# Optimization experiments

Measured on AMD Instinct MI355X. Metric: run time of the kernel, lower is better.

## Reference

```python
import jax, jax.numpy as jnp
import numpy as np

B, TOPK, MN = 128, 32, 64
MAX_NODES, H, E = 256, 128, 128
N_ENT, N_REL = 40000, 400


def setup_inputs() -> dict:
    key = jax.random.key(0)
    ks = jax.random.split(key, 11)
    s = 0.02  # weight init scale
    return {
        "node_embeddings": jax.random.normal(ks[0], (B, MAX_NODES + 2, H), jnp.float32),
        "entity_table": jax.random.normal(ks[1], (N_ENT, E), jnp.float32) * s,
        "relation_table": jax.random.normal(ks[2], (N_REL, E), jnp.float32) * s,
        "W_ih": jax.random.normal(ks[3], (3 * H, 2 * E), jnp.float32) * s,
        "W_hh": jax.random.normal(ks[4], (3 * H, H), jnp.float32) * s,
        "b_ih": jax.random.normal(ks[5], (3 * H,), jnp.float32) * s,
        "b_hh": jax.random.normal(ks[6], (3 * H,), jnp.float32) * s,
        "aim_nodes": jax.random.randint(ks[7], (B, TOPK), 0, MAX_NODES),
        "aim_entities": jax.random.randint(ks[8], (B, TOPK), 0, N_ENT),
        "neighbors": jax.random.randint(ks[9], (B, TOPK, MN, 2), 0, MAX_NODES + 2),
        "neighbors_num": jax.random.randint(ks[10], (B, TOPK), 0, MN + 1),
    }


def reference(node_embeddings, entity_table, relation_table, W_ih, W_hh, b_ih, b_hh,
              aim_nodes, aim_entities, neighbors, neighbors_num):
    # Agent.aggregate with use_rnn=True; returns updated node_embeddings.
    b, topk, mn, _ = neighbors.shape
    h_dim = node_embeddings.shape[-1]
    nb_nodes = neighbors[..., 0]      # (B, topk, mn) node positions
    nb_rel = neighbors[..., 1]        # (B, topk, mn) relation ids

    # per-batch gather of hidden states of neighbor nodes -> (B, topk, mn, H)
    h = jnp.take_along_axis(node_embeddings,
                            nb_nodes.reshape(b, topk * mn)[:, :, None],
                            axis=1).reshape(b, topk, mn, h_dim)
    ent = entity_table[aim_entities]          # (B, topk, E)
    rel = relation_table[nb_rel]              # (B, topk, mn, E)
    # GRU input: concat(aim entity embedding broadcast over neighbors, relation emb)
    x = jnp.concatenate(
        [jnp.broadcast_to(ent[:, :, None, :], rel.shape), rel], axis=-1)  # (B,topk,mn,2E)

    # torch GRUCell: gates ordered (r, z, n)
    gi = jnp.einsum('btme,ge->btmg', x, W_ih) + b_ih  # (B,topk,mn,3H)
    gh = jnp.einsum('btmh,gh->btmg', h, W_hh) + b_hh
    i_r, i_z, i_n = jnp.split(gi, 3, axis=-1)
    h_r, h_z, h_n = jnp.split(gh, 3, axis=-1)
    r = jax.nn.sigmoid(i_r + h_r)
    z = jax.nn.sigmoid(i_z + h_z)
    n = jnp.tanh(i_n + r * h_n)
    h_new = (1.0 - z) * n + z * h              # (B,topk,mn,H)

    # masked mean over valid neighbors (masked_fill(0) then sum / max(num,1))
    mask = jnp.arange(mn)[None, None, :] < neighbors_num[:, :, None]
    denom = neighbors_num.astype(h_new.dtype) + (neighbors_num == 0).astype(h_new.dtype)
    upd = jnp.where(mask[..., None], h_new, 0.0).sum(axis=2) / denom[..., None]  # (B,topk,H)

    # scatter updated representations back into the node table
    bidx = jnp.arange(b)[:, None]
    return node_embeddings.at[bidx, aim_nodes].set(upd)
```

## Files before the change

### kernel.cpp

```cpp
#include <hip/hip_runtime.h>

#define BB     128
#define TOPK   32
#define MN     64
#define NODES  258
#define HD     128
#define G3     384
#define NREL   400
#define SEG1_OFF 448
#define SEG2_OFF 4544
#define NROWS_TOT 37568
#define ROWPAD   37632
#define COLSPLIT 3

typedef __bf16 bf16x8 __attribute__((ext_vector_type(8)));
typedef float  f32x4  __attribute__((ext_vector_type(4)));

__device__ inline unsigned short f2bf(float f) {
    unsigned u = __float_as_uint(f);
    u = (u + 0x7fff + ((u >> 16) & 1)) >> 16;
    return (unsigned short)u;
}
__device__ inline float bf2f(unsigned short s) {
    return __uint_as_float(((unsigned)s) << 16);
}
__device__ inline float fsig(float x) {
    float e = __builtin_amdgcn_exp2f(-1.442695041f * x);
    return __builtin_amdgcn_rcpf(1.f + e);
}
__device__ inline float ftanh(float x) {
    x = fminf(15.f, fmaxf(-15.f, x));
    float e = __builtin_amdgcn_exp2f(2.885390082f * x);
    return (e - 1.f) * __builtin_amdgcn_rcpf(e + 1.f);
}

__global__ __launch_bounds__(256) void pack_all(
        const float* __restrict__ node_emb, const float* __restrict__ ent_tab,
        const float* __restrict__ rel_tab, const int* __restrict__ aim_ent,
        unsigned short* __restrict__ A, float* __restrict__ out) {
    int i = blockIdx.x * 256 + threadIdx.x;
    int row = i >> 4, kc = (i & 15) << 3;
    float4 v0 = {0.f,0.f,0.f,0.f}, v1 = {0.f,0.f,0.f,0.f};
    if (row < NREL) {
        const float4* p = (const float4*)(rel_tab + (size_t)row * 128 + kc);
        v0 = p[0]; v1 = p[1];
    } else if (row < SEG1_OFF) {
    } else if (row < SEG2_OFF) {
        const float* e = ent_tab + (size_t)aim_ent[row - SEG1_OFF] * 128 + kc;
        v0 = ((const float4*)e)[0]; v1 = ((const float4*)e)[1];
    } else if (row < NROWS_TOT) {
        int n = row - SEG2_OFF;
        const float4* p = (const float4*)(node_emb + (size_t)n * 128 + kc);
        v0 = p[0]; v1 = p[1];
        float4* o = (float4*)(out + (size_t)n * 128 + kc);
        o[0] = v0; o[1] = v1;
    }
    union { unsigned short s[8]; uint4 v; } u;
    u.s[0]=f2bf(v0.x); u.s[1]=f2bf(v0.y); u.s[2]=f2bf(v0.z); u.s[3]=f2bf(v0.w);
    u.s[4]=f2bf(v1.x); u.s[5]=f2bf(v1.y); u.s[6]=f2bf(v1.z); u.s[7]=f2bf(v1.w);
    *(uint4*)(A + (size_t)row * 128 + kc) = u.v;
}

__global__ __launch_bounds__(256) void pack_w(
        const float* __restrict__ W_ih, const float* __restrict__ W_hh,
        const float* __restrict__ b_ih, const float* __restrict__ b_hh,
        unsigned short* __restrict__ Wpack, float* __restrict__ biasb) {
    int i = blockIdx.x * 256 + threadIdx.x;
    int s = i / 49152, r = i % 49152;
    int n = r >> 7, k = r & 127;
    float v;
    if (s == 0)      v = W_ih[n * 256 + 128 + k];
    else if (s == 1) v = W_ih[n * 256 + k];
    else             v = W_hh[n * 128 + k];
    Wpack[i] = f2bf(v);
    if (i < 3 * 384) {
        int s2 = i / 384, g = i % 384;
        biasb[i] = (s2 == 0) ? 0.f : (s2 == 1 ? b_ih[g] : b_hh[g]);
    }
}

__global__ __launch_bounds__(256) void mfma_gemm(
        const unsigned short* __restrict__ A, const unsigned short* __restrict__ Wpack,
        const float* __restrict__ biasb, unsigned short* __restrict__ G) {
    __shared__ __align__(16) unsigned short Bs[128 * 128];
    const int tid = threadIdx.x;
    const int w = tid >> 6, lane = tid & 63;
    const int rb = blockIdx.x / COLSPLIT, cs = blockIdx.x % COLSPLIT;
    const int row0 = rb * 128 + w * 32;
    const int seg  = (row0 < SEG1_OFF) ? 0 : (row0 < SEG2_OFF ? 1 : 2);
    const int limit = (seg == 0) ? NREL : NROWS_TOT;
    const int colbase = cs * 128;
    const unsigned short* Wt = Wpack + (size_t)seg * 49152 + (size_t)colbase * 128;

#pragma unroll
    for (int ii = 0; ii < 8; ++ii) {
        int dst = ii * 256 + tid;
        int g = dst >> 6, rem = dst & 63;
        int qq = rem >> 4, cc = rem & 15;
        int tt = g >> 2, kbb = g & 3;
        uint4 v = *(const uint4*)(Wt + (size_t)(tt * 16 + cc) * 128 + kbb * 32 + qq * 8);
        *(uint4*)(Bs + dst * 8) = v;
    }

    const int q = lane >> 4, c = lane & 15;
    const int koff = q << 3;
    bf16x8 a0[4], a1[4];
    {
        const unsigned short* Ar0 = A + (size_t)(row0 + c) * 128 + koff;
        const unsigned short* Ar1 = Ar0 + 16 * 128;
#pragma unroll
        for (int kb = 0; kb < 4; ++kb) {
            a0[kb] = *(const bf16x8*)(Ar0 + kb * 32);
            a1[kb] = *(const bf16x8*)(Ar1 + kb * 32);
        }
    }
    float bv[8];
#pragma unroll
    for (int t = 0; t < 8; ++t)
        bv[t] = biasb[seg * 384 + colbase + t * 16 + c];

    __syncthreads();

    const int r0 = row0 + q * 4, r1 = r0 + 16;
#pragma unroll 2
    for (int t = 0; t < 8; ++t) {
        bf16x8 bf[4];
#pragma unroll
        for (int kb = 0; kb < 4; ++kb)
            bf[kb] = *(const bf16x8*)(Bs + (size_t)((t * 4 + kb) * 64 + lane) * 8);
        f32x4 acc0 = {0.f,0.f,0.f,0.f}, acc1 = {0.f,0.f,0.f,0.f};
#pragma unroll
        for (int kb = 0; kb < 4; ++kb) {
            acc0 = __builtin_amdgcn_mfma_f32_16x16x32_bf16(a0[kb], bf[kb], acc0, 0, 0, 0);
            acc1 = __builtin_amdgcn_mfma_f32_16x16x32_bf16(a1[kb], bf[kb], acc1, 0, 0, 0);
        }
        const int gc = colbase + t * 16 + c;
#pragma unroll
        for (int i2 = 0; i2 < 4; ++i2) {
            if (r0 + i2 < limit) G[(size_t)(r0 + i2) * 384 + gc] = f2bf(acc0[i2] + bv[t]);
            if (r1 + i2 < limit) G[(size_t)(r1 + i2) * 384 + gc] = f2bf(acc1[i2] + bv[t]);
        }
    }
}

__global__ __launch_bounds__(128) void gru_agg(
        const float* __restrict__ node_emb, const unsigned short* __restrict__ G,
        const int* __restrict__ aim_nodes, const int* __restrict__ neighbors,
        const int* __restrict__ nb_num, float* __restrict__ out) {
    const int bt = blockIdx.x;
    const int b = bt >> 5, t = bt & 31;
    const int h = threadIdx.x;

    const int myaim = aim_nodes[bt];
    for (int t2 = t + 1; t2 < TOPK; ++t2)
        if (aim_nodes[b * TOPK + t2] == myaim) return;

    __shared__ int2 nbs[MN];
    if (h < MN) nbs[h] = ((const int2*)(neighbors + (size_t)bt * MN * 2))[h];
    __syncthreads();

    const size_t erow = (size_t)(SEG1_OFF + bt) * 384;
    const float ge_r = bf2f(G[erow + h]);
    const float ge_z = bf2f(G[erow + 128 + h]);
    const float ge_n = bf2f(G[erow + 256 + h]);

    int num = nb_num[bt];
    num = (num < 0) ? 0 : (num > MN ? MN : num);

    const unsigned short* ghb = G + (size_t)(SEG2_OFF + b * NODES) * 384;
    const float* heb = node_emb + (size_t)b * NODES * 128;

    float acc = 0.f;
    int m = 0;
    for (; m + 4 <= num; m += 4) {
        float gr_r[4], gr_z[4], gr_n[4], h_r[4], h_z[4], h_n[4], hv[4];
#pragma unroll
        for (int j = 0; j < 4; ++j) {
            int2 p = nbs[m + j];
            const unsigned short* gr = G + (size_t)p.y * 384;
            const unsigned short* gh = ghb + (size_t)p.x * 384;
            gr_r[j] = bf2f(gr[h]); gr_z[j] = bf2f(gr[128 + h]); gr_n[j] = bf2f(gr[256 + h]);
            h_r[j]  = bf2f(gh[h]); h_z[j]  = bf2f(gh[128 + h]); h_n[j]  = bf2f(gh[256 + h]);
            hv[j]   = heb[(size_t)p.x * 128 + h];
        }
#pragma unroll
        for (int j = 0; j < 4; ++j) {
            float r = fsig(ge_r + gr_r[j] + h_r[j]);
            float z = fsig(ge_z + gr_z[j] + h_z[j]);
            float n = ftanh(ge_n + gr_n[j] + r * h_n[j]);
            acc += (1.f - z) * n + z * hv[j];
        }
    }
    for (; m < num; ++m) {
        int2 p = nbs[m];
        const unsigned short* gr = G + (size_t)p.y * 384;
        const unsigned short* gh = ghb + (size_t)p.x * 384;
        float r = fsig(ge_r + bf2f(gr[h]) + bf2f(gh[h]));
        float z = fsig(ge_z + bf2f(gr[128 + h]) + bf2f(gh[128 + h]));
        float n = ftanh(ge_n + bf2f(gr[256 + h]) + r * bf2f(gh[256 + h]));
        acc += (1.f - z) * n + z * heb[(size_t)p.x * 128 + h];
    }
    const float denom = (num > 0) ? (float)num : 1.f;
    out[((size_t)b * NODES + myaim) * 128 + h] = acc * __builtin_amdgcn_rcpf(denom);
}

extern "C" void kernel_launch(void* const* d_in, const int* in_sizes, int n_in,
                              void* d_out, int out_size, void* d_ws, size_t ws_size,
                              hipStream_t stream) {
    const float* node_emb = (const float*)d_in[0];
    const float* ent_tab  = (const float*)d_in[1];
    const float* rel_tab  = (const float*)d_in[2];
    const float* W_ih     = (const float*)d_in[3];
    const float* W_hh     = (const float*)d_in[4];
    const float* b_ih     = (const float*)d_in[5];
    const float* b_hh     = (const float*)d_in[6];
    const int* aim_nodes  = (const int*)d_in[7];
    const int* aim_ent    = (const int*)d_in[8];
    const int* neighbors  = (const int*)d_in[9];
    const int* nb_num     = (const int*)d_in[10];
    float* out = (float*)d_out;

    unsigned short* G     = (unsigned short*)d_ws;
    unsigned short* A     = G + (size_t)NROWS_TOT * 384;
    unsigned short* Wpack = A + (size_t)ROWPAD * 128;
    float*          biasb = (float*)(Wpack + 3 * 384 * 128);

    hipLaunchKernelGGL(pack_all, dim3(ROWPAD * 16 / 256), dim3(256), 0, stream,
                       node_emb, ent_tab, rel_tab, aim_ent, A, out);
    hipLaunchKernelGGL(pack_w, dim3(3 * 384 * 128 / 256), dim3(256), 0, stream,
                       W_ih, W_hh, b_ih, b_hh, Wpack, biasb);
    hipLaunchKernelGGL(mfma_gemm, dim3((ROWPAD / 128) * COLSPLIT), dim3(256), 0, stream,
                       A, Wpack, biasb, G);
    hipLaunchKernelGGL(gru_agg, dim3(BB * TOPK), dim3(128), 0, stream,
                       node_emb, G, aim_nodes, neighbors, nb_num, out);
}
```

Measured before the change: 151.3 us.

## Split GRU neighbor loop across four thread groups and read bf16 hidden states

The GRU aggregation kernel grows from 128 to 512 threads per block. Each 128-thread group handles every fourth neighbor, and the partial sums are combined through shared memory. This exposes more memory-level parallelism in the latency-bound gathers. The node embeddings are also written to a bf16 copy during packing, so the per-neighbor hidden-state read is halved, at the cost of extra rounding in the z*h term. Segment offsets are realigned to 128-row boundaries so each GEMM block selects a single weight segment.

```diff
diff --git a/kernel.cpp b/kernel.cpp
--- a/kernel.cpp
+++ b/kernel.cpp
@@ -7,9 +7,9 @@
 #define HD     128
 #define G3     384
 #define NREL   400
-#define SEG1_OFF 448
-#define SEG2_OFF 4544
-#define NROWS_TOT 37568
+#define SEG1_OFF 512
+#define SEG2_OFF 4608
+#define NROWS_TOT 37632
 #define ROWPAD   37632
 #define COLSPLIT 3
 
@@ -37,10 +37,13 @@
 __global__ __launch_bounds__(256) void pack_all(
         const float* __restrict__ node_emb, const float* __restrict__ ent_tab,
         const float* __restrict__ rel_tab, const int* __restrict__ aim_ent,
-        unsigned short* __restrict__ A, float* __restrict__ out) {
+        unsigned short* __restrict__ A, unsigned short* __restrict__ NE16,
+        float* __restrict__ out) {
     int i = blockIdx.x * 256 + threadIdx.x;
     int row = i >> 4, kc = (i & 15) << 3;
     float4 v0 = {0.f,0.f,0.f,0.f}, v1 = {0.f,0.f,0.f,0.f};
+    bool isnode = false;
+    int n = 0;
     if (row < NREL) {
         const float4* p = (const float4*)(rel_tab + (size_t)row * 128 + kc);
         v0 = p[0]; v1 = p[1];
@@ -48,8 +51,9 @@
     } else if (row < SEG2_OFF) {
         const float* e = ent_tab + (size_t)aim_ent[row - SEG1_OFF] * 128 + kc;
         v0 = ((const float4*)e)[0]; v1 = ((const float4*)e)[1];
-    } else if (row < NROWS_TOT) {
-        int n = row - SEG2_OFF;
+    } else {
+        isnode = true;
+        n = row - SEG2_OFF;
         const float4* p = (const float4*)(node_emb + (size_t)n * 128 + kc);
         v0 = p[0]; v1 = p[1];
         float4* o = (float4*)(out + (size_t)n * 128 + kc);
@@ -59,6 +63,7 @@
     u.s[0]=f2bf(v0.x); u.s[1]=f2bf(v0.y); u.s[2]=f2bf(v0.z); u.s[3]=f2bf(v0.w);
     u.s[4]=f2bf(v1.x); u.s[5]=f2bf(v1.y); u.s[6]=f2bf(v1.z); u.s[7]=f2bf(v1.w);
     *(uint4*)(A + (size_t)row * 128 + kc) = u.v;
+    if (isnode) *(uint4*)(NE16 + (size_t)n * 128 + kc) = u.v;
 }
 
 __global__ __launch_bounds__(256) void pack_w(
@@ -86,8 +91,9 @@
     const int tid = threadIdx.x;
     const int w = tid >> 6, lane = tid & 63;
     const int rb = blockIdx.x / COLSPLIT, cs = blockIdx.x % COLSPLIT;
-    const int row0 = rb * 128 + w * 32;
-    const int seg  = (row0 < SEG1_OFF) ? 0 : (row0 < SEG2_OFF ? 1 : 2);
+    const int brow = rb * 128;
+    const int row0 = brow + w * 32;
+    const int seg  = (brow < SEG1_OFF) ? 0 : (brow < SEG2_OFF ? 1 : 2);
     const int limit = (seg == 0) ? NREL : NROWS_TOT;
     const int colbase = cs * 128;
     const unsigned short* Wt = Wpack + (size_t)seg * 49152 + (size_t)colbase * 128;
@@ -143,20 +149,22 @@
     }
 }
 
-__global__ __launch_bounds__(128) void gru_agg(
-        const float* __restrict__ node_emb, const unsigned short* __restrict__ G,
+__global__ __launch_bounds__(512) void gru_agg(
+        const unsigned short* __restrict__ NE16, const unsigned short* __restrict__ G,
         const int* __restrict__ aim_nodes, const int* __restrict__ neighbors,
         const int* __restrict__ nb_num, float* __restrict__ out) {
     const int bt = blockIdx.x;
     const int b = bt >> 5, t = bt & 31;
-    const int h = threadIdx.x;
+    const int tid = threadIdx.x;
+    const int h = tid & 127, j = tid >> 7;
 
     const int myaim = aim_nodes[bt];
     for (int t2 = t + 1; t2 < TOPK; ++t2)
         if (aim_nodes[b * TOPK + t2] == myaim) return;
 
     __shared__ int2 nbs[MN];
-    if (h < MN) nbs[h] = ((const int2*)(neighbors + (size_t)bt * MN * 2))[h];
+    __shared__ float part[4][128];
+    if (tid < MN) nbs[tid] = ((const int2*)(neighbors + (size_t)bt * MN * 2))[tid];
     __syncthreads();
 
     const size_t erow = (size_t)(SEG1_OFF + bt) * 384;
@@ -168,40 +176,47 @@
     num = (num < 0) ? 0 : (num > MN ? MN : num);
 
     const unsigned short* ghb = G + (size_t)(SEG2_OFF + b * NODES) * 384;
-    const float* heb = node_emb + (size_t)b * NODES * 128;
+    const unsigned short* heb = NE16 + (size_t)b * NODES * 128;
 
     float acc = 0.f;
-    int m = 0;
-    for (; m + 4 <= num; m += 4) {
-        float gr_r[4], gr_z[4], gr_n[4], h_r[4], h_z[4], h_n[4], hv[4];
-#pragma unroll
-        for (int j = 0; j < 4; ++j) {
-            int2 p = nbs[m + j];
-            const unsigned short* gr = G + (size_t)p.y * 384;
-            const unsigned short* gh = ghb + (size_t)p.x * 384;
-            gr_r[j] = bf2f(gr[h]); gr_z[j] = bf2f(gr[128 + h]); gr_n[j] = bf2f(gr[256 + h]);
-            h_r[j]  = bf2f(gh[h]); h_z[j]  = bf2f(gh[128 + h]); h_n[j]  = bf2f(gh[256 + h]);
-            hv[j]   = heb[(size_t)p.x * 128 + h];
-        }
-#pragma unroll
-        for (int j = 0; j < 4; ++j) {
-            float r = fsig(ge_r + gr_r[j] + h_r[j]);
-            float z = fsig(ge_z + gr_z[j] + h_z[j]);
-            float n = ftanh(ge_n + gr_n[j] + r * h_n[j]);
-            acc += (1.f - z) * n + z * hv[j];
-        }
-    }
-    for (; m < num; ++m) {
+    int m = j;
+    for (; m + 4 < num; m += 8) {
+        int2 p0 = nbs[m], p1 = nbs[m + 4];
+        const unsigned short* gr0 = G + (size_t)p0.y * 384;
+        const unsigned short* gh0 = ghb + (size_t)p0.x * 384;
+        const unsigned short* gr1 = G + (size_t)p1.y * 384;
+        const unsigned short* gh1 = ghb + (size_t)p1.x * 384;
+        float ar0 = bf2f(gr0[h]), az0 = bf2f(gr0[128+h]), an0 = bf2f(gr0[256+h]);
+        float hr0 = bf2f(gh0[h]), hz0 = bf2f(gh0[128+h]), hn0 = bf2f(gh0[256+h]);
+        float hv0 = bf2f(heb[(size_t)p0.x * 128 + h]);
+        float ar1 = bf2f(gr1[h]), az1 = bf2f(gr1[128+h]), an1 = bf2f(gr1[256+h]);
+        float hr1 = bf2f(gh1[h]), hz1 = bf2f(gh1[128+h]), hn1 = bf2f(gh1[256+h]);
+        float hv1 = bf2f(heb[(size_t)p1.x * 128 + h]);
+        float r0 = fsig(ge_r + ar0 + hr0);
+        float z0 = fsig(ge_z + az0 + hz0);
+        float n0 = ftanh(ge_n + an0 + r0 * hn0);
+        acc += (1.f - z0) * n0 + z0 * hv0;
+        float r1 = fsig(ge_r + ar1 + hr1);
+        float z1 = fsig(ge_z + az1 + hz1);
+        float n1 = ftanh(ge_n + an1 + r1 * hn1);
+        acc += (1.f - z1) * n1 + z1 * hv1;
+    }
+    if (m < num) {
         int2 p = nbs[m];
         const unsigned short* gr = G + (size_t)p.y * 384;
         const unsigned short* gh = ghb + (size_t)p.x * 384;
         float r = fsig(ge_r + bf2f(gr[h]) + bf2f(gh[h]));
         float z = fsig(ge_z + bf2f(gr[128 + h]) + bf2f(gh[128 + h]));
         float n = ftanh(ge_n + bf2f(gr[256 + h]) + r * bf2f(gh[256 + h]));
-        acc += (1.f - z) * n + z * heb[(size_t)p.x * 128 + h];
-    }
-    const float denom = (num > 0) ? (float)num : 1.f;
-    out[((size_t)b * NODES + myaim) * 128 + h] = acc * __builtin_amdgcn_rcpf(denom);
+        acc += (1.f - z) * n + z * bf2f(heb[(size_t)p.x * 128 + h]);
+    }
+    part[j][h] = acc;
+    __syncthreads();
+    if (j == 0) {
+        float s = part[0][h] + part[1][h] + part[2][h] + part[3][h];
+        const float denom = (num > 0) ? (float)num : 1.f;
+        out[((size_t)b * NODES + myaim) * 128 + h] = s * __builtin_amdgcn_rcpf(denom);
+    }
 }
 
 extern "C" void kernel_launch(void* const* d_in, const int* in_sizes, int n_in,
@@ -222,15 +237,16 @@
 
     unsigned short* G     = (unsigned short*)d_ws;
     unsigned short* A     = G + (size_t)NROWS_TOT * 384;
-    unsigned short* Wpack = A + (size_t)ROWPAD * 128;
+    unsigned short* NE16  = A + (size_t)ROWPAD * 128;
+    unsigned short* Wpack = NE16 + (size_t)BB * NODES * 128;
     float*          biasb = (float*)(Wpack + 3 * 384 * 128);
 
     hipLaunchKernelGGL(pack_all, dim3(ROWPAD * 16 / 256), dim3(256), 0, stream,
-                       node_emb, ent_tab, rel_tab, aim_ent, A, out);
+                       node_emb, ent_tab, rel_tab, aim_ent, A, NE16, out);
     hipLaunchKernelGGL(pack_w, dim3(3 * 384 * 128 / 256), dim3(256), 0, stream,
                        W_ih, W_hh, b_ih, b_hh, Wpack, biasb);
     hipLaunchKernelGGL(mfma_gemm, dim3((ROWPAD / 128) * COLSPLIT), dim3(256), 0, stream,
                        A, Wpack, biasb, G);
-    hipLaunchKernelGGL(gru_agg, dim3(BB * TOPK), dim3(128), 0, stream,
-                       node_emb, G, aim_nodes, neighbors, nb_num, out);
-}
+    hipLaunchKernelGGL(gru_agg, dim3(BB * TOPK), dim3(512), 0, stream,
+                       NE16, G, aim_nodes, neighbors, nb_num, out);
+}
```

New measurement: 151.2 us. No clear change (-0.1%).

## Fuse node hidden-gate GEMM into GRU aggregation kernel using LDS, merge prep kernels

Applied to the files above, without the earlier changes.

Removes the large global GEMM over all node rows. Each block now computes the W_hh projections for one batch's 258 nodes and a 32-column slice of every gate with MFMA, keeping the results in shared memory instead of writing and re-reading a big bf16 G buffer. The two packing kernels become one launch, and the GEMM kernel now only covers relation and entity rows. The per-node hidden state is read from the bf16 packed A rather than fp32 node_emb, which adds a small precision loss, and the W_hh GEMM work is repeated across the four column-quarter blocks.

```diff
diff --git a/kernel.cpp b/kernel.cpp
--- a/kernel.cpp
+++ b/kernel.cpp
@@ -4,14 +4,13 @@
 #define TOPK   32
 #define MN     64
 #define NODES  258
-#define HD     128
-#define G3     384
+#define NPAD   272
 #define NREL   400
-#define SEG1_OFF 448
-#define SEG2_OFF 4544
-#define NROWS_TOT 37568
-#define ROWPAD   37632
-#define COLSPLIT 3
+#define SEG1_OFF 512
+#define SEG2_OFF 4608
+#define NROWS_TOT 37632
+#define NG_ROWS  4608
+#define GH_STRIDE 102
 
 typedef __bf16 bf16x8 __attribute__((ext_vector_type(8)));
 typedef float  f32x4  __attribute__((ext_vector_type(4)));
@@ -34,61 +33,72 @@
     return (e - 1.f) * __builtin_amdgcn_rcpf(e + 1.f);
 }
 
-__global__ __launch_bounds__(256) void pack_all(
+#define REGA_BLOCKS (NROWS_TOT * 16 / 256)
+#define REGB_BLOCKS (147456 / 8 / 256)
+__global__ __launch_bounds__(256) void prep(
         const float* __restrict__ node_emb, const float* __restrict__ ent_tab,
         const float* __restrict__ rel_tab, const int* __restrict__ aim_ent,
-        unsigned short* __restrict__ A, float* __restrict__ out) {
-    int i = blockIdx.x * 256 + threadIdx.x;
-    int row = i >> 4, kc = (i & 15) << 3;
-    float4 v0 = {0.f,0.f,0.f,0.f}, v1 = {0.f,0.f,0.f,0.f};
-    if (row < NREL) {
-        const float4* p = (const float4*)(rel_tab + (size_t)row * 128 + kc);
-        v0 = p[0]; v1 = p[1];
-    } else if (row < SEG1_OFF) {
-    } else if (row < SEG2_OFF) {
-        const float* e = ent_tab + (size_t)aim_ent[row - SEG1_OFF] * 128 + kc;
-        v0 = ((const float4*)e)[0]; v1 = ((const float4*)e)[1];
-    } else if (row < NROWS_TOT) {
-        int n = row - SEG2_OFF;
-        const float4* p = (const float4*)(node_emb + (size_t)n * 128 + kc);
-        v0 = p[0]; v1 = p[1];
-        float4* o = (float4*)(out + (size_t)n * 128 + kc);
-        o[0] = v0; o[1] = v1;
-    }
-    union { unsigned short s[8]; uint4 v; } u;
-    u.s[0]=f2bf(v0.x); u.s[1]=f2bf(v0.y); u.s[2]=f2bf(v0.z); u.s[3]=f2bf(v0.w);
-    u.s[4]=f2bf(v1.x); u.s[5]=f2bf(v1.y); u.s[6]=f2bf(v1.z); u.s[7]=f2bf(v1.w);
-    *(uint4*)(A + (size_t)row * 128 + kc) = u.v;
-}
-
-__global__ __launch_bounds__(256) void pack_w(
         const float* __restrict__ W_ih, const float* __restrict__ W_hh,
         const float* __restrict__ b_ih, const float* __restrict__ b_hh,
-        unsigned short* __restrict__ Wpack, float* __restrict__ biasb) {
-    int i = blockIdx.x * 256 + threadIdx.x;
-    int s = i / 49152, r = i % 49152;
-    int n = r >> 7, k = r & 127;
-    float v;
-    if (s == 0)      v = W_ih[n * 256 + 128 + k];
-    else if (s == 1) v = W_ih[n * 256 + k];
-    else             v = W_hh[n * 128 + k];
-    Wpack[i] = f2bf(v);
-    if (i < 3 * 384) {
-        int s2 = i / 384, g = i % 384;
-        biasb[i] = (s2 == 0) ? 0.f : (s2 == 1 ? b_ih[g] : b_hh[g]);
-    }
-}
-
-__global__ __launch_bounds__(256) void mfma_gemm(
+        unsigned short* __restrict__ A, unsigned short* __restrict__ Wpack,
+        float* __restrict__ biasb, float* __restrict__ out) {
+    int gid = blockIdx.x * 256 + threadIdx.x;
+    if (blockIdx.x < REGA_BLOCKS) {
+        int row = gid >> 4, kc = (gid & 15) << 3;
+        float4 v0 = {0.f,0.f,0.f,0.f}, v1 = {0.f,0.f,0.f,0.f};
+        if (row < NREL) {
+            const float4* p = (const float4*)(rel_tab + (size_t)row * 128 + kc);
+            v0 = p[0]; v1 = p[1];
+        } else if (row < SEG1_OFF) {
+        } else if (row < SEG2_OFF) {
+            const float* e = ent_tab + (size_t)aim_ent[row - SEG1_OFF] * 128 + kc;
+            v0 = ((const float4*)e)[0]; v1 = ((const float4*)e)[1];
+        } else {
+            int n = row - SEG2_OFF;
+            const float4* p = (const float4*)(node_emb + (size_t)n * 128 + kc);
+            v0 = p[0]; v1 = p[1];
+            float4* o = (float4*)(out + (size_t)n * 128 + kc);
+            o[0] = v0; o[1] = v1;
+        }
+        union { unsigned short s[8]; uint4 v; } u;
+        u.s[0]=f2bf(v0.x); u.s[1]=f2bf(v0.y); u.s[2]=f2bf(v0.z); u.s[3]=f2bf(v0.w);
+        u.s[4]=f2bf(v1.x); u.s[5]=f2bf(v1.y); u.s[6]=f2bf(v1.z); u.s[7]=f2bf(v1.w);
+        *(uint4*)(A + (size_t)row * 128 + kc) = u.v;
+    } else {
+        int rb = gid - REGA_BLOCKS * 256;
+        int e0 = rb * 8;
+        int s = e0 / 49152, r = e0 % 49152;
+        int n = r >> 7, k = r & 127;
+        const float* src = (s == 0) ? (W_ih + n * 256 + 128 + k)
+                         : (s == 1) ? (W_ih + n * 256 + k)
+                                    : (W_hh + n * 128 + k);
+        float4 v0 = ((const float4*)src)[0], v1 = ((const float4*)src)[1];
+        union { unsigned short s[8]; uint4 v; } u;
+        u.s[0]=f2bf(v0.x); u.s[1]=f2bf(v0.y); u.s[2]=f2bf(v0.z); u.s[3]=f2bf(v0.w);
+        u.s[4]=f2bf(v1.x); u.s[5]=f2bf(v1.y); u.s[6]=f2bf(v1.z); u.s[7]=f2bf(v1.w);
+        *(uint4*)(Wpack + e0) = u.v;
+        if (rb < 144) {
+            for (int j = 0; j < 8; ++j) {
+                int e = rb * 8 + j;
+                int s2 = e / 384, g = e % 384;
+                biasb[e] = (s2 == 0) ? 0.f : (s2 == 1 ? b_ih[g] : b_hh[g]);
+            }
+        }
+    }
+}
+
+#define COLSPLIT 3
+__global__ __launch_bounds__(256) void mfma_small(
         const unsigned short* __restrict__ A, const unsigned short* __restrict__ Wpack,
-        const float* __restrict__ biasb, unsigned short* __restrict__ G) {
+        const float* __restrict__ biasb, unsigned short* __restrict__ Gs) {
     __shared__ __align__(16) unsigned short Bs[128 * 128];
     const int tid = threadIdx.x;
     const int w = tid >> 6, lane = tid & 63;
     const int rb = blockIdx.x / COLSPLIT, cs = blockIdx.x % COLSPLIT;
-    const int row0 = rb * 128 + w * 32;
-    const int seg  = (row0 < SEG1_OFF) ? 0 : (row0 < SEG2_OFF ? 1 : 2);
-    const int limit = (seg == 0) ? NREL : NROWS_TOT;
+    const int brow = rb * 128;
+    const int row0 = brow + w * 32;
+    const int seg  = (brow < SEG1_OFF) ? 0 : 1;
+    const int limit = (seg == 0) ? NREL : NG_ROWS;
     const int colbase = cs * 128;
     const unsigned short* Wt = Wpack + (size_t)seg * 49152 + (size_t)colbase * 128;
 
@@ -137,71 +147,108 @@
         const int gc = colbase + t * 16 + c;
 #pragma unroll
         for (int i2 = 0; i2 < 4; ++i2) {
-            if (r0 + i2 < limit) G[(size_t)(r0 + i2) * 384 + gc] = f2bf(acc0[i2] + bv[t]);
-            if (r1 + i2 < limit) G[(size_t)(r1 + i2) * 384 + gc] = f2bf(acc1[i2] + bv[t]);
-        }
-    }
-}
-
-__global__ __launch_bounds__(128) void gru_agg(
-        const float* __restrict__ node_emb, const unsigned short* __restrict__ G,
+            if (r0 + i2 < limit) Gs[(size_t)(r0 + i2) * 384 + gc] = f2bf(acc0[i2] + bv[t]);
+            if (r1 + i2 < limit) Gs[(size_t)(r1 + i2) * 384 + gc] = f2bf(acc1[i2] + bv[t]);
+        }
+    }
+}
+
+__global__ __launch_bounds__(512) void fused_gru(
+        const unsigned short* __restrict__ A, const unsigned short* __restrict__ Wpack,
+        const unsigned short* __restrict__ Gs, const float* __restrict__ b_hh,
         const int* __restrict__ aim_nodes, const int* __restrict__ neighbors,
         const int* __restrict__ nb_num, float* __restrict__ out) {
-    const int bt = blockIdx.x;
-    const int b = bt >> 5, t = bt & 31;
-    const int h = threadIdx.x;
-
-    const int myaim = aim_nodes[bt];
-    for (int t2 = t + 1; t2 < TOPK; ++t2)
-        if (aim_nodes[b * TOPK + t2] == myaim) return;
-
-    __shared__ int2 nbs[MN];
-    if (h < MN) nbs[h] = ((const int2*)(neighbors + (size_t)bt * MN * 2))[h];
+    __shared__ __align__(16) unsigned short gh[NPAD * GH_STRIDE];
+    const int b = blockIdx.x & 127, quart = blockIdx.x >> 7;
+    const int h0 = quart * 32;
+    const int tid = threadIdx.x, w = tid >> 6, lane = tid & 63;
+    const unsigned short* An = A + ((size_t)SEG2_OFF + (size_t)b * NODES) * 128;
+
+    const int q = lane >> 4, c = lane & 15;
+    const int koff = q << 3;
+    const unsigned short* W2 = Wpack + 2 * 49152;
+    for (int rt = w; rt < 17; rt += 8) {
+        int ar = rt * 16 + c;
+        int arc = (ar < NODES) ? ar : 0;
+        bf16x8 af[4];
+#pragma unroll
+        for (int kb = 0; kb < 4; ++kb)
+            af[kb] = *(const bf16x8*)(An + (size_t)arc * 128 + kb * 32 + koff);
+#pragma unroll
+        for (int ct = 0; ct < 6; ++ct) {
+            int gate = ct >> 1, sub = ct & 1;
+            int gc = gate * 128 + h0 + sub * 16 + c;
+            bf16x8 bf[4];
+#pragma unroll
+            for (int kb = 0; kb < 4; ++kb)
+                bf[kb] = *(const bf16x8*)(W2 + (size_t)gc * 128 + kb * 32 + koff);
+            f32x4 acc = {0.f,0.f,0.f,0.f};
+#pragma unroll
+            for (int kb = 0; kb < 4; ++kb)
+                acc = __builtin_amdgcn_mfma_f32_16x16x32_bf16(af[kb], bf[kb], acc, 0, 0, 0);
+            float bias = b_hh[gc];
+            int col = gate * 32 + sub * 16 + c;
+#pragma unroll
+            for (int i2 = 0; i2 < 4; ++i2) {
+                int row = rt * 16 + q * 4 + i2;
+                gh[row * GH_STRIDE + col] = f2bf(acc[i2] + bias);
+            }
+        }
+    }
     __syncthreads();
 
-    const size_t erow = (size_t)(SEG1_OFF + bt) * 384;
-    const float ge_r = bf2f(G[erow + h]);
-    const float ge_z = bf2f(G[erow + 128 + h]);
-    const float ge_n = bf2f(G[erow + 256 + h]);
-
-    int num = nb_num[bt];
-    num = (num < 0) ? 0 : (num > MN ? MN : num);
-
-    const unsigned short* ghb = G + (size_t)(SEG2_OFF + b * NODES) * 384;
-    const float* heb = node_emb + (size_t)b * NODES * 128;
-
-    float acc = 0.f;
-    int m = 0;
-    for (; m + 4 <= num; m += 4) {
-        float gr_r[4], gr_z[4], gr_n[4], h_r[4], h_z[4], h_n[4], hv[4];
-#pragma unroll
-        for (int j = 0; j < 4; ++j) {
-            int2 p = nbs[m + j];
-            const unsigned short* gr = G + (size_t)p.y * 384;
-            const unsigned short* gh = ghb + (size_t)p.x * 384;
-            gr_r[j] = bf2f(gr[h]); gr_z[j] = bf2f(gr[128 + h]); gr_n[j] = bf2f(gr[256 + h]);
-            h_r[j]  = bf2f(gh[h]); h_z[j]  = bf2f(gh[128 + h]); h_n[j]  = bf2f(gh[256 + h]);
-            hv[j]   = heb[(size_t)p.x * 128 + h];
-        }
-#pragma unroll
-        for (int j = 0; j < 4; ++j) {
-            float r = fsig(ge_r + gr_r[j] + h_r[j]);
-            float z = fsig(ge_z + gr_z[j] + h_z[j]);
-            float n = ftanh(ge_n + gr_n[j] + r * h_n[j]);
-            acc += (1.f - z) * n + z * hv[j];
-        }
-    }
-    for (; m < num; ++m) {
-        int2 p = nbs[m];
-        const unsigned short* gr = G + (size_t)p.y * 384;
-        const unsigned short* gh = ghb + (size_t)p.x * 384;
-        float r = fsig(ge_r + bf2f(gr[h]) + bf2f(gh[h]));
-        float z = fsig(ge_z + bf2f(gr[128 + h]) + bf2f(gh[128 + h]));
-        float n = ftanh(ge_n + bf2f(gr[256 + h]) + r * bf2f(gh[256 + h]));
-        acc += (1.f - z) * n + z * heb[(size_t)p.x * 128 + h];
-    }
-    const float denom = (num > 0) ? (float)num : 1.f;
-    out[((size_t)b * NODES + myaim) * 128 + h] = acc * __builtin_amdgcn_rcpf(denom);
+    const int half = lane >> 5, hh = lane & 31;
+    for (int ti = 0; ti < 2; ++ti) {
+        const int t = w * 4 + ti * 2 + half;
+        const int bt = b * TOPK + t;
+        const int aim = aim_nodes[bt];
+        bool wr = true;
+        for (int t2 = t + 1; t2 < TOPK; ++t2)
+            if (aim_nodes[b * TOPK + t2] == aim) wr = false;
+        int num = nb_num[bt];
+        num = (num < 0) ? 0 : (num > MN ? MN : num);
+        const int2* nb = (const int2*)neighbors + (size_t)bt * MN;
+        const size_t erow = (size_t)(SEG1_OFF + bt) * 384;
+        const float ge_r = bf2f(Gs[erow + h0 + hh]);
+        const float ge_z = bf2f(Gs[erow + 128 + h0 + hh]);
+        const float ge_n = bf2f(Gs[erow + 256 + h0 + hh]);
+
+        float acc = 0.f;
+        int m = 0;
+        for (; m + 2 <= num; m += 2) {
+            int2 p0 = nb[m], p1 = nb[m + 1];
+            const unsigned short* gr0 = Gs + (size_t)p0.y * 384 + h0;
+            const unsigned short* gr1 = Gs + (size_t)p1.y * 384 + h0;
+            const unsigned short* g0 = gh + p0.x * GH_STRIDE;
+            const unsigned short* g1 = gh + p1.x * GH_STRIDE;
+            float a_r0 = bf2f(gr0[hh]),  a_z0 = bf2f(gr0[128 + hh]), a_n0 = bf2f(gr0[256 + hh]);
+            float h_r0 = bf2f(g0[hh]),   h_z0 = bf2f(g0[32 + hh]),   h_n0 = bf2f(g0[64 + hh]);
+            float hv0  = bf2f(An[(size_t)p0.x * 128 + h0 + hh]);
+            float a_r1 = bf2f(gr1[hh]),  a_z1 = bf2f(gr1[128 + hh]), a_n1 = bf2f(gr1[256 + hh]);
+            float h_r1 = bf2f(g1[hh]),   h_z1 = bf2f(g1[32 + hh]),   h_n1 = bf2f(g1[64 + hh]);
+            float hv1  = bf2f(An[(size_t)p1.x * 128 + h0 + hh]);
+            float r0 = fsig(ge_r + a_r0 + h_r0);
+            float z0 = fsig(ge_z + a_z0 + h_z0);
+            float n0 = ftanh(ge_n + a_n0 + r0 * h_n0);
+            acc += (1.f - z0) * n0 + z0 * hv0;
+            float r1 = fsig(ge_r + a_r1 + h_r1);
+            float z1 = fsig(ge_z + a_z1 + h_z1);
+            float n1 = ftanh(ge_n + a_n1 + r1 * h_n1);
+            acc += (1.f - z1) * n1 + z1 * hv1;
+        }
+        if (m < num) {
+            int2 p = nb[m];
+            const unsigned short* gr = Gs + (size_t)p.y * 384 + h0;
+            const unsigned short* g0 = gh + p.x * GH_STRIDE;
+            float r = fsig(ge_r + bf2f(gr[hh]) + bf2f(g0[hh]));
+            float z = fsig(ge_z + bf2f(gr[128 + hh]) + bf2f(g0[32 + hh]));
+            float n = ftanh(ge_n + bf2f(gr[256 + hh]) + r * bf2f(g0[64 + hh]));
+            acc += (1.f - z) * n + z * bf2f(An[(size_t)p.x * 128 + h0 + hh]);
+        }
+        const float denom = (num > 0) ? (float)num : 1.f;
+        if (wr)
+            out[((size_t)b * NODES + aim) * 128 + h0 + hh] = acc * __builtin_amdgcn_rcpf(denom);
+    }
 }
 
 extern "C" void kernel_launch(void* const* d_in, const int* in_sizes, int n_in,
@@ -220,17 +267,16 @@
     const int* nb_num     = (const int*)d_in[10];
     float* out = (float*)d_out;
 
-    unsigned short* G     = (unsigned short*)d_ws;
-    unsigned short* A     = G + (size_t)NROWS_TOT * 384;
-    unsigned short* Wpack = A + (size_t)ROWPAD * 128;
+    unsigned short* Gs    = (unsigned short*)d_ws;
+    unsigned short* A     = Gs + (size_t)NG_ROWS * 384;
+    unsigned short* Wpack = A + (size_t)NROWS_TOT * 128;
     float*          biasb = (float*)(Wpack + 3 * 384 * 128);
 
-    hipLaunchKernelGGL(pack_all, dim3(ROWPAD * 16 / 256), dim3(256), 0, stream,
-                       node_emb, ent_tab, rel_tab, aim_ent, A, out);
-    hipLaunchKernelGGL(pack_w, dim3(3 * 384 * 128 / 256), dim3(256), 0, stream,
-                       W_ih, W_hh, b_ih, b_hh, Wpack, biasb);
-    hipLaunchKernelGGL(mfma_gemm, dim3((ROWPAD / 128) * COLSPLIT), dim3(256), 0, stream,
-                       A, Wpack, biasb, G);
-    hipLaunchKernelGGL(gru_agg, dim3(BB * TOPK), dim3(128), 0, stream,
-                       node_emb, G, aim_nodes, neighbors, nb_num, out);
-}
+    hipLaunchKernelGGL(prep, dim3(REGA_BLOCKS + REGB_BLOCKS), dim3(256), 0, stream,
+                       node_emb, ent_tab, rel_tab, aim_ent, W_ih, W_hh, b_ih, b_hh,
+                       A, Wpack, biasb, out);
+    hipLaunchKernelGGL(mfma_small, dim3((NG_ROWS / 128) * COLSPLIT), dim3(256), 0, stream,
+                       A, Wpack, biasb, Gs);
+    hipLaunchKernelGGL(fused_gru, dim3(BB * 4), dim3(512), 0, stream,
+                       A, Wpack, Gs, b_hh, aim_nodes, neighbors, nb_num, out);
+}
```

Measured after the change: 179.3 us. 18.5% more time.
